# Optimization experiments

Measured on AMD Instinct MI355X. Metric: run time of the kernel, lower is better.

Reference implementation:

```python
import jax, jax.numpy as jnp
import numpy as np

N_NODES = 100000


def gcn_conv(x, edge_index, W, b, n_nodes):
    # PyG GCNConv: h = x @ W; add self-loops; symmetric normalization; aggregate to dst; + bias
    h = x @ W  # [N, out]
    loop = jnp.arange(n_nodes, dtype=edge_index.dtype)
    src = jnp.concatenate([edge_index[0], loop])
    dst = jnp.concatenate([edge_index[1], loop])
    ones = jnp.ones(src.shape[0], dtype=h.dtype)
    deg = jax.ops.segment_sum(ones, dst, num_segments=n_nodes)  # in-degree incl. self-loop
    dinv = jnp.where(deg > 0, jax.lax.rsqrt(deg), 0.0)
    norm = dinv[src] * dinv[dst]  # [E+N]
    msgs = h[src] * norm[:, None]  # gather + scale
    out = jax.ops.segment_sum(msgs, dst, num_segments=n_nodes)  # scatter-add
    return out + b


def setup_inputs() -> dict:
    key = jax.random.key(0)
    k1, k2, k3, k4 = jax.random.split(key, 4)
    x = jax.random.normal(k1, (N_NODES, 256), dtype=jnp.float32)
    edge_index = jax.random.randint(k2, (2, 3200000), 0, N_NODES, dtype=jnp.int64)
    W1 = jax.random.normal(k3, (256, 64), dtype=jnp.float32) * (1.0 / np.sqrt(256))
    b1 = jnp.zeros((64,), dtype=jnp.float32)
    W2 = jax.random.normal(k4, (64, 40), dtype=jnp.float32) * (1.0 / np.sqrt(64))
    b2 = jnp.zeros((40,), dtype=jnp.float32)
    return {"x": x, "edge_index": edge_index, "W1": W1, "b1": b1, "W2": W2, "b2": b2}


def reference(x, edge_index, W1, b1, W2, b2):
    n = x.shape[0]
    h = gcn_conv(x, edge_index, W1, b1, n)
    h = jax.nn.relu(h)
    h = gcn_conv(h, edge_index, W2, b2, n)
    return jax.nn.log_softmax(h, axis=1)
```

## Files before the change

### kernel.cpp

```cpp
#include <hip/hip_runtime.h>
#include <hip/hip_bf16.h>
#include <math.h>

static constexpr int NN    = 100000;
static constexpr int BSH   = 9;
static constexpr int NBUCK = (NN + 511) >> 9;
static constexpr int EPB   = 8192;
static constexpr int SCT   = 1024;
static constexpr int CAP   = 24576;

typedef __attribute__((ext_vector_type(8))) short short8;
typedef __attribute__((ext_vector_type(4))) float f32x4;
typedef __attribute__((ext_vector_type(2))) float f32x2;

#if defined(__has_builtin)
#  if __has_builtin(__builtin_amdgcn_cvt_pk_f32_fp8) && __has_builtin(__builtin_amdgcn_cvt_pk_fp8_f32)
#    define USE_HW_FP8 1
#  endif
#endif
#ifndef USE_HW_FP8
#  define USE_HW_FP8 0
#endif

__device__ __forceinline__ short f2bf(float f) {
    __hip_bfloat16 h = __float2bfloat16(f);
    return __builtin_bit_cast(short, h);
}

__device__ __forceinline__ float fp8_dec_sw(unsigned b) {
    unsigned u = ((b & 0x80u) << 24) | ((b & 0x7Fu) << 20);
    return __builtin_bit_cast(float, u) * 0x1p120f;
}
__device__ __forceinline__ unsigned fp8_enc_sw(float f) {
    unsigned u = __builtin_bit_cast(unsigned, f * 0x1p-120f);
    unsigned s = (u >> 24) & 0x80u;
    unsigned mag = u & 0x7FFFFFFFu;
    unsigned t = mag + 0x7FFFFu + ((mag >> 20) & 1u);
    unsigned r = t >> 20;
    if (r > 0x7Eu) r = 0x7Eu;
    return s | r;
}

template<bool HI>
__device__ __forceinline__ f32x2 dec2w(unsigned u) {
#if USE_HW_FP8
    return __builtin_amdgcn_cvt_pk_f32_fp8(u, HI);
#else
    unsigned w = HI ? (u >> 16) : u;
    f32x2 r;
    r.x = fp8_dec_sw(w & 0xFFu);
    r.y = fp8_dec_sw((w >> 8) & 0xFFu);
    return r;
#endif
}
__device__ __forceinline__ unsigned enc2(float a, float b) {
#if USE_HW_FP8
    return (unsigned)__builtin_amdgcn_cvt_pk_fp8_f32(a, b, 0, false);
#else
    return fp8_enc_sw(a) | (fp8_enc_sw(b) << 8);
#endif
}

__device__ __forceinline__ void acc8(f32x2* a, uint2 u) {
    a[0] += dec2w<false>(u.x);
    a[1] += dec2w<true>(u.x);
    a[2] += dec2w<false>(u.y);
    a[3] += dec2w<true>(u.y);
}

__device__ __forceinline__ long long ldidx(const void* __restrict__ p, long long i, int is64) {
    if (is64) return ((const long long* __restrict__)p)[i];
    return (long long)((const int* __restrict__)p)[i];
}

__global__ void k_detect(const unsigned int* __restrict__ e32, int* __restrict__ flag) {
    __shared__ int any_nz;
    if (threadIdx.x == 0) any_nz = 0;
    __syncthreads();
    unsigned int nz = 0;
    for (int w = 1 + 2 * (int)threadIdx.x; w < 4096; w += 512)
        nz |= e32[w];
    if (nz) atomicOr(&any_nz, 1);
    __syncthreads();
    if (threadIdx.x == 0) *flag = (any_nz == 0) ? 1 : 0;
}

__global__ void __launch_bounds__(SCT)
k_scatter_bucket(const void* __restrict__ eidx, const int* __restrict__ flag, long long E,
                 int* __restrict__ gcur, unsigned* __restrict__ ebuf) {
    __shared__ int h[NBUCK];
    for (int b = threadIdx.x; b < NBUCK; b += SCT) h[b] = 0;
    __syncthreads();
    int is64 = *flag;
    long long base = (long long)blockIdx.x * EPB;
    long long end  = base + EPB < E ? base + EPB : E;
    for (long long e = base + threadIdx.x; e < end; e += SCT) {
        int d = (int)ldidx(eidx, E + e, is64);
        atomicAdd(&h[d >> BSH], 1);
    }
    __syncthreads();
    for (int b = threadIdx.x; b < NBUCK; b += SCT)
        h[b] = atomicAdd(&gcur[b], h[b]);
    __syncthreads();
    for (long long e = base + threadIdx.x; e < end; e += SCT) {
        int s = (int)ldidx(eidx, e, is64);
        int d = (int)ldidx(eidx, E + e, is64);
        int bk = d >> BSH;
        int pos = atomicAdd(&h[bk], 1);
        ebuf[(long long)bk * CAP + pos] = (unsigned)s | ((unsigned)(d & 511) << 17);
    }
}

__global__ void k_bucket_starts(const int* __restrict__ gcnt, int* __restrict__ bstart,
                                int* __restrict__ rowst, int n) {
    if (threadIdx.x == 0) {
        int run = 0;
        for (int b = 0; b < NBUCK; ++b) { bstart[b] = run; run += gcnt[b]; }
        bstart[NBUCK] = run;
        rowst[n] = run;
    }
}

__global__ void __launch_bounds__(1024)
k_bucket_csr(const unsigned* __restrict__ ebuf, const int* __restrict__ gcnt,
             const int* __restrict__ bstart, int* __restrict__ rowst,
             float* __restrict__ dinv, int* __restrict__ csr) {
    __shared__ int cnt[512];
    __shared__ int scn[512];
    __shared__ int cursor[512];
    int b = blockIdx.x;
    int t = threadIdx.x;
    int cb = gcnt[b];
    long long rbase = (long long)b * CAP;
    int bs = bstart[b];
    if (t < 512) cnt[t] = 0;
    __syncthreads();
    for (int i = t; i < cb; i += 1024) {
        unsigned ed = ebuf[rbase + i];
        atomicAdd(&cnt[ed >> 17], 1);
    }
    __syncthreads();
    if (t < 512) scn[t] = cnt[t];
    __syncthreads();
    for (int off = 1; off < 512; off <<= 1) {
        int v = 0;
        if (t < 512 && t >= off) v = scn[t - off];
        __syncthreads();
        if (t < 512) scn[t] += v;
        __syncthreads();
    }
    if (t < 512) {
        int start = bs + scn[t] - cnt[t];
        int gnode = (b << BSH) + t;
        if (gnode < NN) {
            rowst[gnode] = start;
            dinv[gnode]  = rsqrtf((float)(cnt[t] + 1));
        }
        cursor[t] = start;
    }
    __syncthreads();
    for (int i = t; i < cb; i += 1024) {
        unsigned ed = ebuf[rbase + i];
        int pos = atomicAdd(&cursor[ed >> 17], 1);
        csr[pos] = (int)(ed & 0x1FFFFu);
    }
}

template<int K, int NCOLS, int KT, int NT>
__global__ void k_packB(const float* __restrict__ W, short* __restrict__ P) {
    int t = blockIdx.x * blockDim.x + threadIdx.x;
    if (t >= KT * NT * 64) return;
    int kt = t / (NT * 64);
    int nt = (t / 64) % NT;
    int l  = t & 63;
    int g  = l >> 4;
#pragma unroll
    for (int e = 0; e < 8; ++e) {
        int k   = kt * 32 + g * 8 + e;
        int col = nt * 16 + (l & 15);
        float v = (col < NCOLS) ? W[k * NCOLS + col] : 0.0f;
        P[t * 8 + e] = f2bf(v);
    }
}

template<int K, int NCOLS, int KT, int NT, bool ABF16>
__global__ void __launch_bounds__(256)
k_mfma_gemm(const void* __restrict__ Xv, const short* __restrict__ packedB,
            const float* __restrict__ dinv, unsigned char* __restrict__ H, int n) {
    __shared__ alignas(16) short sW[KT * NT * 512];
    short8* dst = (short8*)sW;
    const short8* src = (const short8*)packedB;
    constexpr int TOT8 = KT * NT * 64;
    for (int i = threadIdx.x; i < TOT8; i += 256) dst[i] = src[i];
    __syncthreads();

    int wave = threadIdx.x >> 6, lane = threadIdx.x & 63;
    int g = lane >> 4;
    int arow = blockIdx.x * 64 + wave * 16 + (lane & 15);

    f32x4 acc[NT];
#pragma unroll
    for (int nt = 0; nt < NT; ++nt) acc[nt] = (f32x4){0.f, 0.f, 0.f, 0.f};

#pragma unroll
    for (int kt = 0; kt < KT; ++kt) {
        short8 a;
        if (arow < n) {
            int k0 = kt * 32 + g * 8;
            if (ABF16) {
                const short* xr = (const short*)Xv + (long long)arow * K;
                a = *(const short8*)(xr + k0);
            } else {
                const float* xr = (const float*)Xv + (long long)arow * K;
                float4 u = *(const float4*)(xr + k0);
                float4 v = *(const float4*)(xr + k0 + 4);
                a[0] = f2bf(u.x); a[1] = f2bf(u.y); a[2] = f2bf(u.z); a[3] = f2bf(u.w);
                a[4] = f2bf(v.x); a[5] = f2bf(v.y); a[6] = f2bf(v.z); a[7] = f2bf(v.w);
            }
        } else {
            a = (short8){0, 0, 0, 0, 0, 0, 0, 0};
        }
#pragma unroll
        for (int nt = 0; nt < NT; ++nt) {
            short8 bfr = dst[(kt * NT + nt) * 64 + lane];
            acc[nt] = __builtin_amdgcn_mfma_f32_16x16x32_bf16(a, bfr, acc[nt], 0, 0, 0);
        }
    }

    int c = lane & 15;
    int orow_base = blockIdx.x * 64 + wave * 16 + g * 4;
#pragma unroll
    for (int r = 0; r < 4; ++r) {
        int orow = orow_base + r;
        if (orow < n) {
            float di = dinv[orow];
            float v[NT];
#pragma unroll
            for (int nt = 0; nt < NT; ++nt) v[nt] = acc[nt][r] * di;
            unsigned char* hp = H + (long long)orow * NCOLS;
#pragma unroll
            for (int p = 0; p < NT; p += 2) {
                unsigned wrd = enc2(v[p], (p + 1 < NT) ? v[p + 1] : 0.0f);
                int col0 = p * 16 + c;
                if (col0 < NCOLS) hp[col0] = (unsigned char)(wrd & 0xFFu);
                if (p + 1 < NT) {
                    int col1 = col0 + 16;
                    if (col1 < NCOLS) hp[col1] = (unsigned char)((wrd >> 8) & 0xFFu);
                }
            }
        }
    }
}

__global__ void __launch_bounds__(256)
k_gather_relu(const int* __restrict__ rowst, const int* __restrict__ csr,
              const unsigned char* __restrict__ h1s, const float* __restrict__ dinv,
              const float* __restrict__ b, unsigned short* __restrict__ out, int n) {
    long long gid = (long long)blockIdx.x * blockDim.x + threadIdx.x;
    int node = (int)(gid >> 3);
    int fe   = (int)(gid & 7);
    if (node >= n) return;
    int jb = rowst[node], je = rowst[node + 1];
    unsigned feoff = (unsigned)fe << 3;

    f32x2 a0[4], a1[4];
#pragma unroll
    for (int q = 0; q < 4; ++q) { a0[q] = (f32x2){0.f, 0.f}; a1[q] = (f32x2){0.f, 0.f}; }

    int j = jb;
    for (; j + 1 < je; j += 2) {
        int s0 = csr[j];
        int s1 = csr[j + 1];
        uint2 u0 = *(const uint2*)(h1s + (((unsigned)s0 << 6) + feoff));
        uint2 u1 = *(const uint2*)(h1s + (((unsigned)s1 << 6) + feoff));
        acc8(a0, u0);
        acc8(a1, u1);
    }
    if (j < je) {
        int s0 = csr[j];
        uint2 u0 = *(const uint2*)(h1s + (((unsigned)s0 << 6) + feoff));
        acc8(a0, u0);
    }
#pragma unroll
    for (int q = 0; q < 4; ++q) a0[q] += a1[q];

    uint2 self = *(const uint2*)(h1s + (((unsigned)node << 6) + feoff));
    acc8(a0, self);
    float di = dinv[node];
    unsigned short r[8];
#pragma unroll
    for (int q = 0; q < 4; ++q) {
        float v0 = fmaxf(a0[q].x * di + b[8 * fe + 2 * q],     0.0f);
        float v1 = fmaxf(a0[q].y * di + b[8 * fe + 2 * q + 1], 0.0f);
        r[2 * q]     = (unsigned short)f2bf(v0);
        r[2 * q + 1] = (unsigned short)f2bf(v1);
    }
    uint4 pk;
    pk.x = (unsigned)r[0] | ((unsigned)r[1] << 16);
    pk.y = (unsigned)r[2] | ((unsigned)r[3] << 16);
    pk.z = (unsigned)r[4] | ((unsigned)r[5] << 16);
    pk.w = (unsigned)r[6] | ((unsigned)r[7] << 16);
    ((uint4*)(out + (long long)node * 64))[fe] = pk;
}

__global__ void __launch_bounds__(256)
k_gather_lsm(const int* __restrict__ rowst, const int* __restrict__ csr,
             const unsigned char* __restrict__ h2s, const float* __restrict__ dinv,
             const float* __restrict__ b, float* __restrict__ out, int n) {
    long long gid = (long long)blockIdx.x * blockDim.x + threadIdx.x;
    int node = (int)(gid >> 3);
    int fe   = (int)(gid & 7);
    if (node >= n) return;
    bool act = (fe < 5);
    int jb = rowst[node], je = rowst[node + 1];
    unsigned feoff = (unsigned)fe << 3;

    f32x2 a0[4], a1[4];
#pragma unroll
    for (int q = 0; q < 4; ++q) { a0[q] = (f32x2){0.f, 0.f}; a1[q] = (f32x2){0.f, 0.f}; }

    int j = jb;
    for (; j + 1 < je; j += 2) {
        int s0 = csr[j];
        int s1 = csr[j + 1];
        if (act) {
            uint2 u0 = *(const uint2*)(h2s + ((unsigned)s0 * 40u + feoff));
            uint2 u1 = *(const uint2*)(h2s + ((unsigned)s1 * 40u + feoff));
            acc8(a0, u0);
            acc8(a1, u1);
        }
    }
    if (j < je && act) {
        int s0 = csr[j];
        uint2 u0 = *(const uint2*)(h2s + ((unsigned)s0 * 40u + feoff));
        acc8(a0, u0);
    }
#pragma unroll
    for (int q = 0; q < 4; ++q) a0[q] += a1[q];

    float va[8];
    float mloc = -INFINITY;
    if (act) {
        uint2 self = *(const uint2*)(h2s + ((unsigned)node * 40u + feoff));
        acc8(a0, self);
        float di = dinv[node];
#pragma unroll
        for (int q = 0; q < 4; ++q) {
            va[2 * q]     = a0[q].x * di + b[8 * fe + 2 * q];
            va[2 * q + 1] = a0[q].y * di + b[8 * fe + 2 * q + 1];
            mloc = fmaxf(mloc, fmaxf(va[2 * q], va[2 * q + 1]));
        }
    }
    float m = mloc;
    m = fmaxf(m, __shfl_xor(m, 1));
    m = fmaxf(m, __shfl_xor(m, 2));
    m = fmaxf(m, __shfl_xor(m, 4));
    float ex = 0.0f;
    if (act) {
#pragma unroll
        for (int k = 0; k < 8; ++k) ex += __expf(va[k] - m);
    }
    ex += __shfl_xor(ex, 1);
    ex += __shfl_xor(ex, 2);
    ex += __shfl_xor(ex, 4);
    float lse = __logf(ex);
    if (act) {
        float4 r0 = make_float4(va[0] - m - lse, va[1] - m - lse,
                                va[2] - m - lse, va[3] - m - lse);
        float4 r1 = make_float4(va[4] - m - lse, va[5] - m - lse,
                                va[6] - m - lse, va[7] - m - lse);
        *(float4*)(out + (long long)node * 40 + 8 * fe)     = r0;
        *(float4*)(out + (long long)node * 40 + 8 * fe + 4) = r1;
    }
}

extern "C" void kernel_launch(void* const* d_in, const int* in_sizes, int n_in,
                              void* d_out, int out_size, void* d_ws, size_t ws_size,
                              hipStream_t stream) {
    const float* x  = (const float*)d_in[0];
    const void*  ei = d_in[1];
    const float* W1 = (const float*)d_in[2];
    const float* b1 = (const float*)d_in[3];
    const float* W2 = (const float*)d_in[4];
    const float* b2 = (const float*)d_in[5];
    float* out = (float*)d_out;

    const long long E = (long long)in_sizes[1] / 2;
    const int nblk = (int)((E + EPB - 1) / EPB);

    char* w = (char*)d_ws;
    auto alloc = [&](size_t bytes) -> void* {
        void* p = (void*)w;
        w += (bytes + 255) & ~(size_t)255;
        return p;
    };
    int*      flag    = (int*)     alloc(4);
    int*      gcur    = (int*)     alloc((size_t)NBUCK * 4);
    int*      bstart  = (int*)     alloc(((size_t)NBUCK + 1) * 4);
    int*      rowst   = (int*)     alloc(((size_t)NN + 1) * 4);
    float*    dinv    = (float*)   alloc((size_t)NN * 4);
    short*    pB1     = (short*)   alloc((size_t)8 * 4 * 64 * 8 * 2);
    short*    pB2     = (short*)   alloc((size_t)2 * 3 * 64 * 8 * 2);
    int*      csr     = (int*)     alloc((size_t)E * 4);
    unsigned* ebuf    = (unsigned*)alloc((size_t)NBUCK * CAP * 4);
    unsigned short* agg1 = (unsigned short*)alloc((size_t)NN * 64 * 2);
    unsigned char* h1s = (unsigned char*)ebuf;
    unsigned char* h2s = h1s;

    const int B = 256;
    auto cdiv = [](long long a, long long b) { return (int)((a + b - 1) / b); };

    k_detect<<<1, 256, 0, stream>>>((const unsigned int*)ei, flag);
    k_packB<256, 64, 8, 4><<<cdiv(8 * 4 * 64, B), B, 0, stream>>>(W1, pB1);
    k_packB<64, 40, 2, 3><<<cdiv(2 * 3 * 64, B), B, 0, stream>>>(W2, pB2);

    hipMemsetAsync(gcur, 0, (size_t)NBUCK * 4, stream);
    k_scatter_bucket<<<nblk, SCT, 0, stream>>>(ei, flag, E, gcur, ebuf);
    k_bucket_starts<<<1, 64, 0, stream>>>(gcur, bstart, rowst, NN);
    k_bucket_csr<<<NBUCK, 1024, 0, stream>>>(ebuf, gcur, bstart, rowst, dinv, csr);

    k_mfma_gemm<256, 64, 8, 4, false><<<cdiv(NN, 64), B, 0, stream>>>(x, pB1, dinv, h1s, NN);

    k_gather_relu<<<cdiv((long long)NN * 8, B), B, 0, stream>>>(rowst, csr, h1s, dinv, b1, agg1, NN);

    k_mfma_gemm<64, 40, 2, 3, true><<<cdiv(NN, 64), B, 0, stream>>>(agg1, pB2, dinv, h2s, NN);

    k_gather_lsm<<<cdiv((long long)NN * 8, B), B, 0, stream>>>(rowst, csr, h2s, dinv, b2, out, NN);
}
```

Measured before the change: 203.2 us.

## Merge init kernels, cache edge loads in registers, use wave-shuffle scan

Fuses the index-width detection, the two weight-packing kernels and the bucket-counter memset into one 11-block launch, which removes several small launches. The scatter kernel now keeps each thread's eight source/destination indices in registers between the histogram pass and the placement pass instead of reading edge_index twice from global memory. The per-bucket prefix scan drops its 9-step shared-memory Hillis-Steele loop in favour of a wave shuffle scan plus a small cross-wave combine, cutting the number of block barriers. Register use rises, and the unroll assumes EPB equals 8*SCT.

```diff
diff --git a/kernel.cpp b/kernel.cpp
--- a/kernel.cpp
+++ b/kernel.cpp
@@ -73,16 +73,45 @@
     return (long long)((const int* __restrict__)p)[i];
 }
 
-__global__ void k_detect(const unsigned int* __restrict__ e32, int* __restrict__ flag) {
-    __shared__ int any_nz;
-    if (threadIdx.x == 0) any_nz = 0;
-    __syncthreads();
-    unsigned int nz = 0;
-    for (int w = 1 + 2 * (int)threadIdx.x; w < 4096; w += 512)
-        nz |= e32[w];
-    if (nz) atomicOr(&any_nz, 1);
-    __syncthreads();
-    if (threadIdx.x == 0) *flag = (any_nz == 0) ? 1 : 0;
+template<int K, int NCOLS, int KT, int NT>
+__device__ __forceinline__ void packB_dev(const float* __restrict__ W,
+                                          short* __restrict__ P, int t) {
+    if (t >= KT * NT * 64) return;
+    int kt = t / (NT * 64);
+    int nt = (t / 64) % NT;
+    int l  = t & 63;
+    int g  = l >> 4;
+#pragma unroll
+    for (int e = 0; e < 8; ++e) {
+        int k   = kt * 32 + g * 8 + e;
+        int col = nt * 16 + (l & 15);
+        float v = (col < NCOLS) ? W[k * NCOLS + col] : 0.0f;
+        P[t * 8 + e] = f2bf(v);
+    }
+}
+
+__global__ void __launch_bounds__(256)
+k_init(const unsigned int* __restrict__ e32, int* __restrict__ flag,
+       int* __restrict__ gcur,
+       const float* __restrict__ W1, short* __restrict__ pB1,
+       const float* __restrict__ W2, short* __restrict__ pB2) {
+    int blk = blockIdx.x, tid = threadIdx.x;
+    if (blk == 0) {
+        if (tid < NBUCK) gcur[tid] = 0;
+        __shared__ int any_nz;
+        if (tid == 0) any_nz = 0;
+        __syncthreads();
+        unsigned int nz = 0;
+        for (int w = 1 + 2 * tid; w < 4096; w += 512)
+            nz |= e32[w];
+        if (nz) atomicOr(&any_nz, 1);
+        __syncthreads();
+        if (tid == 0) *flag = (any_nz == 0) ? 1 : 0;
+    } else if (blk <= 8) {
+        packB_dev<256, 64, 8, 4>(W1, pB1, (blk - 1) * 256 + tid);
+    } else {
+        packB_dev<64, 40, 2, 3>(W2, pB2, (blk - 9) * 256 + tid);
+    }
 }
 
 __global__ void __launch_bounds__(SCT)
@@ -94,20 +123,29 @@
     int is64 = *flag;
     long long base = (long long)blockIdx.x * EPB;
     long long end  = base + EPB < E ? base + EPB : E;
-    for (long long e = base + threadIdx.x; e < end; e += SCT) {
-        int d = (int)ldidx(eidx, E + e, is64);
-        atomicAdd(&h[d >> BSH], 1);
+    unsigned sv[8], dv[8];
+    bool ok[8];
+#pragma unroll
+    for (int k = 0; k < 8; ++k) {
+        long long e = base + (long long)k * SCT + threadIdx.x;
+        ok[k] = (e < end);
+        if (ok[k]) {
+            sv[k] = (unsigned)ldidx(eidx, e, is64);
+            dv[k] = (unsigned)ldidx(eidx, E + e, is64);
+            atomicAdd(&h[dv[k] >> BSH], 1);
+        }
     }
     __syncthreads();
     for (int b = threadIdx.x; b < NBUCK; b += SCT)
         h[b] = atomicAdd(&gcur[b], h[b]);
     __syncthreads();
-    for (long long e = base + threadIdx.x; e < end; e += SCT) {
-        int s = (int)ldidx(eidx, e, is64);
-        int d = (int)ldidx(eidx, E + e, is64);
-        int bk = d >> BSH;
-        int pos = atomicAdd(&h[bk], 1);
-        ebuf[(long long)bk * CAP + pos] = (unsigned)s | ((unsigned)(d & 511) << 17);
+#pragma unroll
+    for (int k = 0; k < 8; ++k) {
+        if (ok[k]) {
+            int bk = dv[k] >> BSH;
+            int pos = atomicAdd(&h[bk], 1);
+            ebuf[(long long)bk * CAP + pos] = sv[k] | ((dv[k] & 511u) << 17);
+        }
     }
 }
 
@@ -126,8 +164,8 @@
              const int* __restrict__ bstart, int* __restrict__ rowst,
              float* __restrict__ dinv, int* __restrict__ csr) {
     __shared__ int cnt[512];
-    __shared__ int scn[512];
     __shared__ int cursor[512];
+    __shared__ int woff[8];
     int b = blockIdx.x;
     int t = threadIdx.x;
     int cb = gcnt[b];
@@ -140,21 +178,32 @@
         atomicAdd(&cnt[ed >> 17], 1);
     }
     __syncthreads();
-    if (t < 512) scn[t] = cnt[t];
-    __syncthreads();
-    for (int off = 1; off < 512; off <<= 1) {
-        int v = 0;
-        if (t < 512 && t >= off) v = scn[t - off];
-        __syncthreads();
-        if (t < 512) scn[t] += v;
-        __syncthreads();
-    }
+    int v = 0, ps = 0;
     if (t < 512) {
-        int start = bs + scn[t] - cnt[t];
+        v = cnt[t];
+        ps = v;
+        int lane = t & 63;
+#pragma unroll
+        for (int off = 1; off < 64; off <<= 1) {
+            int up = __shfl_up(ps, off);
+            if (lane >= off) ps += up;
+        }
+        if (lane == 63) woff[t >> 6] = ps;
+    }
+    __syncthreads();
+    if (t == 0) {
+        int run = 0;
+#pragma unroll
+        for (int i = 0; i < 8; ++i) { int x = woff[i]; woff[i] = run; run += x; }
+    }
+    __syncthreads();
+    if (t < 512) {
+        int incl  = ps + woff[t >> 6];
+        int start = bs + incl - v;
         int gnode = (b << BSH) + t;
         if (gnode < NN) {
             rowst[gnode] = start;
-            dinv[gnode]  = rsqrtf((float)(cnt[t] + 1));
+            dinv[gnode]  = rsqrtf((float)(v + 1));
         }
         cursor[t] = start;
     }
@@ -163,23 +212,6 @@
         unsigned ed = ebuf[rbase + i];
         int pos = atomicAdd(&cursor[ed >> 17], 1);
         csr[pos] = (int)(ed & 0x1FFFFu);
-    }
-}
-
-template<int K, int NCOLS, int KT, int NT>
-__global__ void k_packB(const float* __restrict__ W, short* __restrict__ P) {
-    int t = blockIdx.x * blockDim.x + threadIdx.x;
-    if (t >= KT * NT * 64) return;
-    int kt = t / (NT * 64);
-    int nt = (t / 64) % NT;
-    int l  = t & 63;
-    int g  = l >> 4;
-#pragma unroll
-    for (int e = 0; e < 8; ++e) {
-        int k   = kt * 32 + g * 8 + e;
-        int col = nt * 16 + (l & 15);
-        float v = (col < NCOLS) ? W[k * NCOLS + col] : 0.0f;
-        P[t * 8 + e] = f2bf(v);
     }
 }
 
@@ -410,11 +442,8 @@
     const int B = 256;
     auto cdiv = [](long long a, long long b) { return (int)((a + b - 1) / b); };
 
-    k_detect<<<1, 256, 0, stream>>>((const unsigned int*)ei, flag);
-    k_packB<256, 64, 8, 4><<<cdiv(8 * 4 * 64, B), B, 0, stream>>>(W1, pB1);
-    k_packB<64, 40, 2, 3><<<cdiv(2 * 3 * 64, B), B, 0, stream>>>(W2, pB2);
-
-    hipMemsetAsync(gcur, 0, (size_t)NBUCK * 4, stream);
+    k_init<<<11, B, 0, stream>>>((const unsigned int*)ei, flag, gcur, W1, pB1, W2, pB2);
+
     k_scatter_bucket<<<nblk, SCT, 0, stream>>>(ei, flag, E, gcur, ebuf);
     k_bucket_starts<<<1, 64, 0, stream>>>(gcur, bstart, rowst, NN);
     k_bucket_csr<<<NBUCK, 1024, 0, stream>>>(ebuf, gcur, bstart, rowst, dinv, csr);
```

Result: faster. 193.4 us (-4.8%).
